# Kernel optimization log

Hardware: AMD Instinct MI355X
Metric: run time of the kernel (lower is better)

The kernel has to match this reference:

```python
import jax, jax.numpy as jnp
import numpy as np

OUT_FEATURES = 1024
DELTA = 0.1
# 32 groups, each with multiplicity 16 -> in_features = 512
CONFIGURE = [(f"g{i}", 16) for i in range(32)]

# Reproduce the original forward's weight-expansion (including the inner-loop
# index shadowing: a group with count k>1 stacks weight rows 0..k-1).
def _row_index():
    idx = []
    for i, (_, k) in enumerate(CONFIGURE):
        if k == 1:
            idx.append(np.array([i]))
        else:
            idx.append(np.arange(k))
    return np.concatenate(idx)

ROW_IDX = jnp.asarray(_row_index())          # (in_features,)
IN_FEATURES = int(ROW_IDX.shape[0])          # 512


def setup_inputs() -> dict:
    key = jax.random.key(0)
    k1, k2 = jax.random.split(key)
    x = jax.random.normal(k1, (128, IN_FEATURES), dtype=jnp.float32)
    # nn.init.normal_(std=0.1) on a (n_groups, out_features) parameter
    weights = 0.1 * jax.random.normal(k2, (len(CONFIGURE), OUT_FEATURES), dtype=jnp.float32)
    return {"x": x, "weights": weights}


def reference(x, weights):
    W = weights[ROW_IDX]                         # (in, out) expanded per-group weights
    # fused elementwise multiply + abs, then dual reduction over in_features
    abs_w = jnp.abs(W[None, :, :] * x[:, :, None])   # (B, in, out)
    bias = jnp.max(abs_w, axis=1) - jnp.sum(abs_w, axis=1)  # (B, out)
    # mask broadcasts over out_features, so masked batched matmul == (x*mask) @ W
    mask = (x >= -1).astype(x.dtype)             # (B, in)
    out = (x * mask) @ W                          # (B, out)
    return out + DELTA * bias
```

## Files before the change

kernel.cpp:

```cpp
#include <hip/hip_runtime.h>

#define IN_F   512
#define OUT_F  1024
#define NR     16
#define NG     32
#define DELTA  0.1f

__global__ __launch_bounds__(1024)
void conj_kernel(const float* __restrict__ x,
                 const float* __restrict__ w,
                 float* __restrict__ out) {
    __shared__ float s_sx[NR];
    __shared__ float s_sxm[NR];
    __shared__ float s_mx[NR];

    const int b = blockIdx.x;
    const int t = threadIdx.x;

    if (t < IN_F) {
        const int r = t >> 5;
        const int g = t & 31;
        const float xv = x[b * IN_F + g * NR + r];
        const float ax = fabsf(xv);
        const float xm = (xv >= -1.0f) ? xv : 0.0f;

        float sx = ax, sm = xm, mx = ax;
        #pragma unroll
        for (int m = 16; m >= 1; m >>= 1) {
            sx += __shfl_xor(sx, m);
            sm += __shfl_xor(sm, m);
            mx = fmaxf(mx, __shfl_xor(mx, m));
        }
        if (g == 0) {
            s_sx[r]  = sx;
            s_sxm[r] = sm;
            s_mx[r]  = mx;
        }
    }
    __syncthreads();

    const int o = t;
    float acc = 0.0f;
    float sab = 0.0f;
    float mxv = 0.0f;
    #pragma unroll
    for (int r = 0; r < NR; ++r) {
        const float wv = w[r * OUT_F + o];
        const float aw = fabsf(wv);
        acc += wv * s_sxm[r];
        sab += aw * s_sx[r];
        mxv = fmaxf(mxv, aw * s_mx[r]);
    }
    out[b * OUT_F + o] = acc + DELTA * (mxv - sab);
}

extern "C" void kernel_launch(void* const* d_in, const int* in_sizes, int n_in,
                              void* d_out, int out_size, void* d_ws, size_t ws_size,
                              hipStream_t stream) {
    const float* x = (const float*)d_in[0];
    const float* w = (const float*)d_in[1];
    float* out = (float*)d_out;
    conj_kernel<<<128, 1024, 0, stream>>>(x, w, out);
}
```

Before: 10.62 us.

## Split work into single-wave blocks and replace shared-memory reduction with shuffles

Launches one 64-thread wave per (batch row, 64-output chunk) instead of one 1024-thread block per row. Each wave redundantly reduces its x row by residue using register accumulation and cross-lane shuffles, removing shared memory and the block barrier. Weight loads are issued up front to overlap with the reduction. This trades redundant x reads (16x per row, cached) for more blocks and no synchronization.

```diff
diff --git a/kernel.cpp b/kernel.cpp
--- a/kernel.cpp
+++ b/kernel.cpp
@@ -3,53 +3,54 @@
 #define IN_F   512
 #define OUT_F  1024
 #define NR     16
-#define NG     32
 #define DELTA  0.1f
 
-__global__ __launch_bounds__(1024)
+__global__ __launch_bounds__(64)
 void conj_kernel(const float* __restrict__ x,
                  const float* __restrict__ w,
                  float* __restrict__ out) {
-    __shared__ float s_sx[NR];
-    __shared__ float s_sxm[NR];
-    __shared__ float s_mx[NR];
+    const int bid   = blockIdx.x;
+    const int b     = bid >> 4;
+    const int chunk = bid & 15;
+    const int l     = threadIdx.x;
+    const int o     = chunk * 64 + l;
 
-    const int b = blockIdx.x;
-    const int t = threadIdx.x;
+    float wv[NR];
+    #pragma unroll
+    for (int r = 0; r < NR; ++r)
+        wv[r] = w[r * OUT_F + o];
 
-    if (t < IN_F) {
-        const int r = t >> 5;
-        const int g = t & 31;
-        const float xv = x[b * IN_F + g * NR + r];
+    const float* xrow = x + b * IN_F;
+    float sx = 0.0f;
+    float sm = 0.0f;
+    float mx = 0.0f;
+    #pragma unroll
+    for (int k = 0; k < 8; ++k) {
+        const float xv = xrow[l + 64 * k];
         const float ax = fabsf(xv);
-        const float xm = (xv >= -1.0f) ? xv : 0.0f;
+        sx += ax;
+        sm += (xv >= -1.0f) ? xv : 0.0f;
+        mx = fmaxf(mx, ax);
+    }
+    sx += __shfl_xor(sx, 16);
+    sm += __shfl_xor(sm, 16);
+    mx = fmaxf(mx, __shfl_xor(mx, 16));
+    sx += __shfl_xor(sx, 32);
+    sm += __shfl_xor(sm, 32);
+    mx = fmaxf(mx, __shfl_xor(mx, 32));
 
-        float sx = ax, sm = xm, mx = ax;
-        #pragma unroll
-        for (int m = 16; m >= 1; m >>= 1) {
-            sx += __shfl_xor(sx, m);
-            sm += __shfl_xor(sm, m);
-            mx = fmaxf(mx, __shfl_xor(mx, m));
-        }
-        if (g == 0) {
-            s_sx[r]  = sx;
-            s_sxm[r] = sm;
-            s_mx[r]  = mx;
-        }
-    }
-    __syncthreads();
-
-    const int o = t;
     float acc = 0.0f;
     float sab = 0.0f;
     float mxv = 0.0f;
     #pragma unroll
     for (int r = 0; r < NR; ++r) {
-        const float wv = w[r * OUT_F + o];
-        const float aw = fabsf(wv);
-        acc += wv * s_sxm[r];
-        sab += aw * s_sx[r];
-        mxv = fmaxf(mxv, aw * s_mx[r]);
+        const float sm_r = __shfl(sm, r);
+        const float sx_r = __shfl(sx, r);
+        const float mx_r = __shfl(mx, r);
+        const float aw = fabsf(wv[r]);
+        acc += wv[r] * sm_r;
+        sab += aw * sx_r;
+        mxv = fmaxf(mxv, aw * mx_r);
     }
     out[b * OUT_F + o] = acc + DELTA * (mxv - sab);
 }
@@ -60,5 +61,5 @@
     const float* x = (const float*)d_in[0];
     const float* w = (const float*)d_in[1];
     float* out = (float*)d_out;
-    conj_kernel<<<128, 1024, 0, stream>>>(x, w, out);
+    conj_kernel<<<2048, 64, 0, stream>>>(x, w, out);
 }
```

Measured after the change: 9.373 us. -11.7%, faster.
